# Optimization experiments

Measured on AMD Instinct MI355X. Metric: run time of the kernel, lower is better.

The kernel has to match this reference:

```python
import jax, jax.numpy as jnp
import numpy as np


def setup_inputs() -> dict:
    key = jax.random.key(0)
    k1, k2, k3 = jax.random.split(key, 3)
    l, p, m, n = 8, 1, 4096, 1024
    inp = jax.random.normal(k1, (l, p, m, n), dtype=jnp.float32)
    alpha = jax.random.uniform(k2, (1,), dtype=jnp.float32, minval=0.001, maxval=1.0)
    beta = jax.random.uniform(k3, (1,), dtype=jnp.float32, minval=0.001, maxval=1.0)
    return {"input": inp, "alpha": alpha, "beta": beta}


def reference(input, alpha, beta):
    # w[0] = 1; w[k] = w[k-1] + alpha / w[k-1] - beta * input[..., k-1]
    l, p, m, n = input.shape
    a = alpha[0]
    b = beta[0]
    # scan over the last axis: move it to leading axis; only first n-1 inputs drive the recurrence
    xs = jnp.moveaxis(input[..., : n - 1], -1, 0)  # (n-1, l, p, m)
    w0 = jnp.ones((l, p, m), dtype=input.dtype)

    def step(w, x):
        w_next = w + a / w - b * x
        return w_next, w_next

    _, ws = jax.lax.scan(step, w0, xs)  # (n-1, l, p, m)
    wm = jnp.concatenate([w0[None], ws], axis=0)  # (n, l, p, m)
    wm = jnp.moveaxis(wm, 0, -1)  # (l, p, m, n)
    return wm.reshape(l, m * n)  # valid because p == 1
```

## Files before the change

### kernel.cpp

```cpp
#include <hip/hip_runtime.h>


#define N_COLS 1024
#define DC 32
#define NDC 32
#define RING 8
#define ROWS 64
#define SLOTF 2048

#define WAITVM(n) asm volatile("s_waitcnt vmcnt(" #n ")" ::: "memory")
#define WAITLGKM0() asm volatile("s_waitcnt lgkmcnt(0)" ::: "memory")
#define BARRIER() __builtin_amdgcn_s_barrier()

__device__ __forceinline__ float fdiv_rn_exact(float a, float w) {
    float d, n, r0, e, r1, q, e2, q1, e3, f, res;
    unsigned long long sj;
    asm volatile(
        "v_div_scale_f32 %[d], vcc, %[w], %[w], %[a]\n\t"
        "v_div_scale_f32 %[n], %[sj], %[a], %[w], %[a]\n\t"
        "v_rcp_f32 %[r0], %[d]\n\t"
        "s_nop 1\n\t"
        "v_fma_f32 %[e], -%[d], %[r0], 1.0\n\t"
        "v_fma_f32 %[r1], %[e], %[r0], %[r0]\n\t"
        "v_mul_f32 %[q], %[n], %[r1]\n\t"
        "v_fma_f32 %[e2], -%[d], %[q], %[n]\n\t"
        "v_fma_f32 %[q1], %[e2], %[r1], %[q]\n\t"
        "v_fma_f32 %[e3], -%[d], %[q1], %[n]\n\t"
        "v_div_fmas_f32 %[f], %[e3], %[r1], %[q1]\n\t"
        "v_div_fixup_f32 %[res], %[f], %[w], %[a]"
        : [d] "=&v"(d), [n] "=&v"(n), [r0] "=&v"(r0), [e] "=&v"(e),
          [r1] "=&v"(r1), [q] "=&v"(q), [e2] "=&v"(e2), [q1] "=&v"(q1),
          [e3] "=&v"(e3), [f] "=&v"(f), [res] "=v"(res), [sj] "=&s"(sj)
        : [a] "v"(a), [w] "v"(w)
        : "vcc");
    return res;
}

__device__ __forceinline__ float stepf(float w, float x, float a, float b) {
    return __fsub_rn(__fadd_rn(w, fdiv_rn_exact(a, w)), __fmul_rn(b, x));
}

__global__ __launch_bounds__(192) void DDK_77644418777662_kernel(
    const float* __restrict__ in, float* __restrict__ out,
    const float* __restrict__ alpha, const float* __restrict__ beta,
    int n_rows) {
    __shared__ float ibuf[RING * SLOTF];
    __shared__ float obuf[2 * SLOTF];

    const int tid = threadIdx.x;
    const int wid = tid >> 6;
    const int lane = tid & 63;
    const int row_base = blockIdx.x * ROWS;
    if (row_base >= n_rows) return;

    const int lr = lane >> 3;
    const int cg = (lane & 7) ^ lr;

    if (wid == 1) {
        const float* src0 = in + (size_t)(row_base + lr) * N_COLS + cg * 4;

#define STAGE_AT(S, C) do {                                                    \
    float* dst_ = ibuf + (S) * SLOTF;                                          \
    const float* s_ = src0 + (C) * DC;                                         \
    _Pragma("unroll")                                                          \
    for (int q_ = 0; q_ < 8; ++q_) {                                           \
        __builtin_amdgcn_global_load_lds(                                      \
            (const __attribute__((address_space(1))) void*)(s_ + (size_t)q_ * 8 * N_COLS), \
            (__attribute__((address_space(3))) void*)(dst_ + q_ * 256), 16, 0, 0);         \
    }                                                                          \
} while (0)

        WAITVM(0);
        STAGE_AT(0, 0); STAGE_AT(1, 1); STAGE_AT(2, 2); STAGE_AT(3, 3);
        STAGE_AT(4, 4); STAGE_AT(5, 5); STAGE_AT(6, 6);
        WAITVM(48);

#pragma unroll 1
        for (int c = 0; c < NDC; ++c) {
            BARRIER();
            if (c <= NDC - RING) {
                STAGE_AT((c + 7) & 7, c + 7);
                WAITVM(48);
            } else if (c == 25) { WAITVM(40); }
            else if (c == 26) { WAITVM(32); }
            else if (c == 27) { WAITVM(24); }
            else if (c == 28) { WAITVM(16); }
            else if (c == 29) { WAITVM(8); }
            else if (c == 30) { WAITVM(0); }
        }
        BARRIER();
#undef STAGE_AT

    } else if (wid == 2) {
        float* dst0 = out + (size_t)(row_base + lr) * N_COLS + cg * 4;

#define STORE_CHUNK(C) do {                                                    \
    const float* ob_ = obuf + ((C) & 1) * SLOTF;                               \
    float4 v_[8];                                                              \
    _Pragma("unroll")                                                          \
    for (int q_ = 0; q_ < 8; ++q_)                                             \
        v_[q_] = *(const float4*)(ob_ + q_ * 256 + lane * 4);                  \
    WAITLGKM0();                                                               \
    _Pragma("unroll")                                                          \
    for (int q_ = 0; q_ < 8; ++q_)                                             \
        *(float4*)(dst0 + (size_t)q_ * 8 * N_COLS + (C) * DC) = v_[q_];        \
} while (0)

#pragma unroll 1
        for (int c = 0; c < NDC; ++c) {
            BARRIER();
            if (c >= 1) STORE_CHUNK(c - 1);
        }
        BARRIER();
        STORE_CHUNK(NDC - 1);
#undef STORE_CHUNK

    } else {
        const float a = alpha[0];
        const float b = beta[0];

        const int q = lane >> 3, h = lane & 7;
        const int base_f = q * 256 + h * 32;
        int off[8];
#pragma unroll
        for (int g = 0; g < 8; ++g) off[g] = base_f + ((g ^ h) * 4);

        float w = 1.0f;
#pragma unroll 1
        for (int c = 0; c < NDC; ++c) {
            BARRIER();
            const float* ib = ibuf + (c & 7) * SLOTF;
            float4 v[8];
#pragma unroll
            for (int g = 0; g < 8; ++g) v[g] = *(const float4*)(ib + off[g]);
            float x[32];
#pragma unroll
            for (int g = 0; g < 8; ++g) {
                x[g * 4 + 0] = v[g].x; x[g * 4 + 1] = v[g].y;
                x[g * 4 + 2] = v[g].z; x[g * 4 + 3] = v[g].w;
            }
            float o[32];
            o[0] = w;
#pragma unroll
            for (int i = 1; i < 32; ++i) { w = stepf(w, x[i - 1], a, b); o[i] = w; }
            w = stepf(w, x[31], a, b);

            float* ob = obuf + (c & 1) * SLOTF;
#pragma unroll
            for (int g = 0; g < 8; ++g)
                *(float4*)(ob + off[g]) = make_float4(o[g * 4 + 0], o[g * 4 + 1],
                                                      o[g * 4 + 2], o[g * 4 + 3]);
            WAITLGKM0();
        }
        BARRIER();
    }
}

extern "C" void kernel_launch(void* const* d_in, const int* in_sizes, int n_in,
                              void* d_out, int out_size, void* d_ws, size_t ws_size,
                              hipStream_t stream) {
    const float* in = (const float*)d_in[0];
    const float* alpha = (const float*)d_in[1];
    const float* beta = (const float*)d_in[2];
    float* out = (float*)d_out;

    int total = in_sizes[0];
    int n_rows = total / N_COLS;

    dim3 grid(n_rows / ROWS);
    dim3 block(192);
    DDK_77644418777662_kernel<<<grid, block, 0, stream>>>(in, out, alpha, beta,
                                                          n_rows);
}
```

Measured before the change: 271.0 us.

## Restructure warp-specialized pipeline with four loader warps and two storer warps

Replaces the one-loader/one-storer/one-compute warp layout with four loader warps, one compute warp and two store warps (448 threads). Input is staged in large double-buffered events of 128 columns across 64 rows, and compute runs in 64-column groups with a double barrier per group. The aim is more memory-level parallelism and fewer, larger transfers per barrier. In exchange the loader now waits for vmcnt(0) in a coarse double-buffer instead of an 8-deep ring, which risks exposing load latency to the serial compute warp. The larger block and shared-memory footprint also reduce occupancy.

```diff
diff --git a/kernel.cpp b/kernel.cpp
--- a/kernel.cpp
+++ b/kernel.cpp
@@ -2,13 +2,9 @@
 
 
 #define N_COLS 1024
-#define DC 32
-#define NDC 32
-#define RING 8
-#define ROWS 64
-#define SLOTF 2048
+#define NG 16
 
-#define WAITVM(n) asm volatile("s_waitcnt vmcnt(" #n ")" ::: "memory")
+#define WAITVM0() asm volatile("s_waitcnt vmcnt(0)" ::: "memory")
 #define WAITLGKM0() asm volatile("s_waitcnt lgkmcnt(0)" ::: "memory")
 #define BARRIER() __builtin_amdgcn_s_barrier()
 
@@ -40,119 +36,144 @@
     return __fsub_rn(__fadd_rn(w, fdiv_rn_exact(a, w)), __fmul_rn(b, x));
 }
 
-__global__ __launch_bounds__(192) void DDK_77644418777662_kernel(
+__global__ __launch_bounds__(448) void DDK_77644418777662_kernel(
     const float* __restrict__ in, float* __restrict__ out,
     const float* __restrict__ alpha, const float* __restrict__ beta,
     int n_rows) {
-    __shared__ float ibuf[RING * SLOTF];
-    __shared__ float obuf[2 * SLOTF];
+    __shared__ float ibuf[2 * 8192];
+    __shared__ float obuf[4096];
 
     const int tid = threadIdx.x;
     const int wid = tid >> 6;
     const int lane = tid & 63;
-    const int row_base = blockIdx.x * ROWS;
+    const int row_base = blockIdx.x * 64;
     if (row_base >= n_rows) return;
 
-    const int lr = lane >> 3;
-    const int cg = (lane & 7) ^ lr;
+    if (wid >= 1 && wid <= 4) {
+        const int lw = wid - 1;
+        const int rsub = lw * 2 + (lane >> 5);
+        const int u = lane & 31;
+        const int pu = (u & 16) | ((u & 15) ^ rsub);
+        const float* srcb = in + (size_t)(row_base + rsub) * N_COLS + pu * 4;
 
-    if (wid == 1) {
-        const float* src0 = in + (size_t)(row_base + lr) * N_COLS + cg * 4;
-
-#define STAGE_AT(S, C) do {                                                    \
-    float* dst_ = ibuf + (S) * SLOTF;                                          \
-    const float* s_ = src0 + (C) * DC;                                         \
+#define ISSUE_EVENT(E) do {                                                    \
+    const int q_ = (E) & 1;                                                    \
     _Pragma("unroll")                                                          \
-    for (int q_ = 0; q_ < 8; ++q_) {                                           \
+    for (int k_ = 0; k_ < 8; ++k_) {                                           \
         __builtin_amdgcn_global_load_lds(                                      \
-            (const __attribute__((address_space(1))) void*)(s_ + (size_t)q_ * 8 * N_COLS), \
-            (__attribute__((address_space(3))) void*)(dst_ + q_ * 256), 16, 0, 0);         \
+            (const __attribute__((address_space(1))) void*)                    \
+                (srcb + (E) * 128 + k_ * 8192),                                \
+            (__attribute__((address_space(3))) void*)                          \
+                (ibuf + q_ * 8192 + k_ * 1024 + lw * 256),                     \
+            16, 0, 0);                                                         \
     }                                                                          \
 } while (0)
 
-        WAITVM(0);
-        STAGE_AT(0, 0); STAGE_AT(1, 1); STAGE_AT(2, 2); STAGE_AT(3, 3);
-        STAGE_AT(4, 4); STAGE_AT(5, 5); STAGE_AT(6, 6);
-        WAITVM(48);
+        WAITVM0();
+        ISSUE_EVENT(0);
+        WAITVM0();
+        BARRIER();
+#pragma unroll 1
+        for (int g = 0; g <= NG; ++g) {
+            BARRIER();
+            BARRIER();
+            if ((g & 1) == 0) {
+                int p = (g >> 1) + 1;
+                if (p <= 7) ISSUE_EVENT(p);
+            } else if (g <= 13) {
+                WAITVM0();
+            }
+        }
+#undef ISSUE_EVENT
 
+    } else if (wid == 0) {
+        const float a = alpha[0];
+        const float b = beta[0];
+        const int c = lane & 7;
+        float* ob = obuf + lane * 64;
+
+        float w = 1.0f;
+        BARRIER();
 #pragma unroll 1
-        for (int c = 0; c < NDC; ++c) {
+        for (int g = 0; g <= NG; ++g) {
             BARRIER();
-            if (c <= NDC - RING) {
-                STAGE_AT((c + 7) & 7, c + 7);
-                WAITVM(48);
-            } else if (c == 25) { WAITVM(40); }
-            else if (c == 26) { WAITVM(32); }
-            else if (c == 27) { WAITVM(24); }
-            else if (c == 28) { WAITVM(16); }
-            else if (c == 29) { WAITVM(8); }
-            else if (c == 30) { WAITVM(0); }
+            BARRIER();
+            if (g < NG) {
+                const float* ib = ibuf + ((g >> 1) & 1) * 8192 + lane * 128 +
+                                  (g & 1) * 64;
+                float4 x0 = *(const float4*)(ib + ((0 ^ c) << 2));
+                float4 x1 = *(const float4*)(ib + ((1 ^ c) << 2));
+                float4 x2 = *(const float4*)(ib + ((2 ^ c) << 2));
+                float4 x3 = *(const float4*)(ib + ((3 ^ c) << 2));
+                float4 x4 = *(const float4*)(ib + ((4 ^ c) << 2));
+                float4 x5 = *(const float4*)(ib + ((5 ^ c) << 2));
+                float4 x6 = *(const float4*)(ib + ((6 ^ c) << 2));
+                float4 x7 = *(const float4*)(ib + ((7 ^ c) << 2));
+                float4 x8 = *(const float4*)(ib + ((8 ^ c) << 2));
+                float4 x9 = *(const float4*)(ib + ((9 ^ c) << 2));
+                float4 xa = *(const float4*)(ib + ((10 ^ c) << 2));
+                float4 xb_ = *(const float4*)(ib + ((11 ^ c) << 2));
+                float4 xc_ = *(const float4*)(ib + ((12 ^ c) << 2));
+                float4 xd = *(const float4*)(ib + ((13 ^ c) << 2));
+                float4 xe = *(const float4*)(ib + ((14 ^ c) << 2));
+                float4 xf = *(const float4*)(ib + ((15 ^ c) << 2));
+
+#define UNITSTEP(W_, XU) do {                                                  \
+    float4 o_;                                                                 \
+    o_.x = w; w = stepf(w, XU.x, a, b);                                        \
+    o_.y = w; w = stepf(w, XU.y, a, b);                                        \
+    o_.z = w; w = stepf(w, XU.z, a, b);                                        \
+    o_.w = w; w = stepf(w, XU.w, a, b);                                        \
+    *(float4*)(ob + (((W_) ^ c) << 2)) = o_;                                   \
+} while (0)
+                UNITSTEP(0, x0);  UNITSTEP(1, x1);  UNITSTEP(2, x2);
+                UNITSTEP(3, x3);  UNITSTEP(4, x4);  UNITSTEP(5, x5);
+                UNITSTEP(6, x6);  UNITSTEP(7, x7);  UNITSTEP(8, x8);
+                UNITSTEP(9, x9);  UNITSTEP(10, xa); UNITSTEP(11, xb_);
+                UNITSTEP(12, xc_); UNITSTEP(13, xd); UNITSTEP(14, xe);
+                UNITSTEP(15, xf);
+#undef UNITSTEP
+                WAITLGKM0();
+            }
         }
-        BARRIER();
-#undef STAGE_AT
-
-    } else if (wid == 2) {
-        float* dst0 = out + (size_t)(row_base + lr) * N_COLS + cg * 4;
-
-#define STORE_CHUNK(C) do {                                                    \
-    const float* ob_ = obuf + ((C) & 1) * SLOTF;                               \
-    float4 v_[8];                                                              \
-    _Pragma("unroll")                                                          \
-    for (int q_ = 0; q_ < 8; ++q_)                                             \
-        v_[q_] = *(const float4*)(ob_ + q_ * 256 + lane * 4);                  \
-    WAITLGKM0();                                                               \
-    _Pragma("unroll")                                                          \
-    for (int q_ = 0; q_ < 8; ++q_)                                             \
-        *(float4*)(dst0 + (size_t)q_ * 8 * N_COLS + (C) * DC) = v_[q_];        \
-} while (0)
-
-#pragma unroll 1
-        for (int c = 0; c < NDC; ++c) {
-            BARRIER();
-            if (c >= 1) STORE_CHUNK(c - 1);
-        }
-        BARRIER();
-        STORE_CHUNK(NDC - 1);
-#undef STORE_CHUNK
 
     } else {
-        const float a = alpha[0];
-        const float b = beta[0];
+        const int sw = wid - 5;
+        const int rsub = sw * 4 + (lane >> 4);
+        const int j = lane & 15;
+        const int m = j ^ rsub;
+        const float* obb = obuf + rsub * 64 + m * 4;
+        float* dstb = out + (size_t)(row_base + rsub) * N_COLS + j * 4;
 
-        const int q = lane >> 3, h = lane & 7;
-        const int base_f = q * 256 + h * 32;
-        int off[8];
-#pragma unroll
-        for (int g = 0; g < 8; ++g) off[g] = base_f + ((g ^ h) * 4);
-
-        float w = 1.0f;
+        BARRIER();
 #pragma unroll 1
-        for (int c = 0; c < NDC; ++c) {
+        for (int g = 0; g <= NG; ++g) {
             BARRIER();
-            const float* ib = ibuf + (c & 7) * SLOTF;
-            float4 v[8];
-#pragma unroll
-            for (int g = 0; g < 8; ++g) v[g] = *(const float4*)(ib + off[g]);
-            float x[32];
-#pragma unroll
-            for (int g = 0; g < 8; ++g) {
-                x[g * 4 + 0] = v[g].x; x[g * 4 + 1] = v[g].y;
-                x[g * 4 + 2] = v[g].z; x[g * 4 + 3] = v[g].w;
+            float4 v0, v1, v2, v3, v4, v5, v6, v7;
+            if (g >= 1) {
+                v0 = *(const float4*)(obb + 0 * 512);
+                v1 = *(const float4*)(obb + 1 * 512);
+                v2 = *(const float4*)(obb + 2 * 512);
+                v3 = *(const float4*)(obb + 3 * 512);
+                v4 = *(const float4*)(obb + 4 * 512);
+                v5 = *(const float4*)(obb + 5 * 512);
+                v6 = *(const float4*)(obb + 6 * 512);
+                v7 = *(const float4*)(obb + 7 * 512);
+                WAITLGKM0();
             }
-            float o[32];
-            o[0] = w;
-#pragma unroll
-            for (int i = 1; i < 32; ++i) { w = stepf(w, x[i - 1], a, b); o[i] = w; }
-            w = stepf(w, x[31], a, b);
-
-            float* ob = obuf + (c & 1) * SLOTF;
-#pragma unroll
-            for (int g = 0; g < 8; ++g)
-                *(float4*)(ob + off[g]) = make_float4(o[g * 4 + 0], o[g * 4 + 1],
-                                                      o[g * 4 + 2], o[g * 4 + 3]);
-            WAITLGKM0();
+            BARRIER();
+            if (g >= 1) {
+                float* d = dstb + (size_t)(g - 1) * 64;
+                *(float4*)(d + 0 * 8192) = v0;
+                *(float4*)(d + 1 * 8192) = v1;
+                *(float4*)(d + 2 * 8192) = v2;
+                *(float4*)(d + 3 * 8192) = v3;
+                *(float4*)(d + 4 * 8192) = v4;
+                *(float4*)(d + 5 * 8192) = v5;
+                *(float4*)(d + 6 * 8192) = v6;
+                *(float4*)(d + 7 * 8192) = v7;
+            }
         }
-        BARRIER();
     }
 }
 
@@ -167,8 +188,8 @@
     int total = in_sizes[0];
     int n_rows = total / N_COLS;
 
-    dim3 grid(n_rows / ROWS);
-    dim3 block(192);
+    dim3 grid(n_rows / 64);
+    dim3 block(448);
     DDK_77644418777662_kernel<<<grid, block, 0, stream>>>(in, out, alpha, beta,
                                                           n_rows);
 }
```

Result: faster. 256.2 us (-5.5%).
